# Kernel optimization log

Measured on AMD Instinct MI355X. Metric: run time of the kernel, lower is better.

## Reference

```python
import jax, jax.numpy as jnp
import numpy as np

N_NODES = 100000
N_EDGES = 1600000
NUM_GRAPHS = 128


def _gcn_layer(x, W, b, senders, receivers, n_node):
    # Linear transform first (cheaper: feature dim small)
    x = x @ W + b  # [N, out]
    ones = jnp.ones(senders.shape[0], dtype=x.dtype)
    deg_s = jax.ops.segment_sum(ones, senders, n_node)     # out-degree
    deg_r = jax.ops.segment_sum(ones, receivers, n_node)   # in-degree
    # symmetric normalization: D^-1/2 A D^-1/2
    x = x * jax.lax.rsqrt(jnp.maximum(deg_s, 1.0))[:, None]
    x = jax.ops.segment_sum(x[senders], receivers, n_node)  # gather-scatter aggregation
    x = x * jax.lax.rsqrt(jnp.maximum(deg_r, 1.0))[:, None]
    return x


def setup_inputs() -> dict:
    key = jax.random.key(0)
    ks = jax.random.split(key, 10)
    x = jax.random.normal(ks[0], (N_NODES, 9), dtype=jnp.float32)
    senders = jax.random.randint(ks[1], (N_EDGES,), 0, N_NODES)
    receivers = jax.random.randint(ks[2], (N_EDGES,), 0, N_NODES)
    batch = jnp.sort(jax.random.randint(ks[3], (N_NODES,), 0, NUM_GRAPHS))
    # learned params (Dense: W [in,out], b [out]) with LeCun-normal-ish scale
    def dense(k, din, dout):
        return jax.random.normal(k, (din, dout), dtype=jnp.float32) / np.sqrt(din)
    W1 = dense(ks[4], 9, 64)
    b1 = jnp.zeros((64,), jnp.float32)
    W2 = dense(ks[5], 64, 128)
    b2 = jnp.zeros((128,), jnp.float32)
    W3 = dense(ks[6], 128, 2)
    b3 = jnp.zeros((2,), jnp.float32)
    return {"x": x, "senders": senders, "receivers": receivers, "batch": batch,
            "num_graphs": NUM_GRAPHS, "W1": W1, "b1": b1, "W2": W2, "b2": b2,
            "W3": W3, "b3": b3}


def reference(x, senders, receivers, batch, num_graphs, W1, b1, W2, b2, W3, b3):
    n_node = x.shape[0]
    x = jax.nn.relu(_gcn_layer(x, W1, b1, senders, receivers, n_node))
    x = jax.nn.relu(_gcn_layer(x, W2, b2, senders, receivers, n_node))
    x = _gcn_layer(x, W3, b3, senders, receivers, n_node)
    # graph-level pooling
    return jax.ops.segment_sum(x, batch, num_graphs)
```

## Files before the change

### kernel.cpp

```cpp
#include <hip/hip_runtime.h>
#include <hip/hip_bf16.h>
#include <cstddef>

#define NBMAX 512
#define BCAP 5120
#define BKCHUNK 3200

typedef unsigned short bf16t;
typedef __attribute__((ext_vector_type(8))) short short8;
typedef __attribute__((ext_vector_type(4))) float f32x4;

static __device__ __forceinline__ float2 up2(unsigned u) {
    return make_float2(__uint_as_float(u << 16), __uint_as_float(u & 0xffff0000u));
}
static __device__ __forceinline__ bf16t f2bf(float f) {
    unsigned u = __float_as_uint(f);
    u += 0x7fffu + ((u >> 16) & 1u);
    return (bf16t)(u >> 16);
}
static __device__ __forceinline__ unsigned pk2(float a, float b) {
    return (unsigned)f2bf(a) | ((unsigned)f2bf(b) << 16);
}

__global__ void k_bucket(const int* __restrict__ S, const int* __restrict__ R,
                         unsigned* __restrict__ bufR, unsigned char* __restrict__ bufS,
                         int* __restrict__ gCntR, int* __restrict__ gCntS,
                         const float* __restrict__ W2, bf16t* __restrict__ W2f,
                         int nE, int nB) {
    __shared__ int histR[NBMAX], lstR[NBMAX], baseR[NBMAX];
    __shared__ int histS[NBMAX], lstS[NBMAX], baseS[NBMAX];
    __shared__ int sm[256];
    __shared__ unsigned sortedR[BKCHUNK];
    __shared__ unsigned short bOfR[BKCHUNK];
    __shared__ unsigned char sortedS[BKCHUNK];
    __shared__ unsigned short bOfS[BKCHUNK];
    int t = threadIdx.x;
    int nSort = gridDim.x - 4;
    if (blockIdx.x >= nSort) {
        int tt = (blockIdx.x - nSort) * blockDim.x + t;
        if (tt < 1024) {
            int nt = tt >> 7, kh = (tt >> 6) & 1, lane = tt & 63;
            int n = nt * 16 + (lane & 15);
            int k0 = kh * 32 + (lane >> 4) * 8;
            uint4 p;
            p.x = pk2(W2[(k0 + 0) * 128 + n], W2[(k0 + 1) * 128 + n]);
            p.y = pk2(W2[(k0 + 2) * 128 + n], W2[(k0 + 3) * 128 + n]);
            p.z = pk2(W2[(k0 + 4) * 128 + n], W2[(k0 + 5) * 128 + n]);
            p.w = pk2(W2[(k0 + 6) * 128 + n], W2[(k0 + 7) * 128 + n]);
            ((uint4*)W2f)[tt] = p;
        }
        return;
    }
    for (int i = t; i < NBMAX; i += 256) { histR[i] = 0; histS[i] = 0; }
    __syncthreads();
    int chunk = (nE + nSort - 1) / nSort;
    int e0 = blockIdx.x * chunk;
    int e1 = min(e0 + chunk, nE);
    for (int e = e0 + t; e < e1; e += 256) {
        atomicAdd(&histR[R[e] >> 8], 1);
        atomicAdd(&histS[S[e] >> 8], 1);
    }
    __syncthreads();
    {
        int c0 = histR[2 * t], c1 = histR[2 * t + 1];
        int ps = c0 + c1;
        sm[t] = ps;
        __syncthreads();
        for (int off = 1; off < 256; off <<= 1) {
            int y = (t >= off) ? sm[t - off] : 0;
            __syncthreads();
            sm[t] += y;
            __syncthreads();
        }
        int ex = sm[t] - ps;
        lstR[2 * t] = ex;
        lstR[2 * t + 1] = ex + c0;
    }
    __syncthreads();
    {
        int c0 = histS[2 * t], c1 = histS[2 * t + 1];
        int ps = c0 + c1;
        sm[t] = ps;
        __syncthreads();
        for (int off = 1; off < 256; off <<= 1) {
            int y = (t >= off) ? sm[t - off] : 0;
            __syncthreads();
            sm[t] += y;
            __syncthreads();
        }
        int ex = sm[t] - ps;
        lstS[2 * t] = ex;
        lstS[2 * t + 1] = ex + c0;
    }
    __syncthreads();
    for (int i = t; i < nB; i += 256) {
        int cR = histR[i];
        baseR[i] = cR ? atomicAdd(&gCntR[i], cR) : 0;
        int cS = histS[i];
        baseS[i] = cS ? atomicAdd(&gCntS[i], cS) : 0;
    }
    for (int i = t; i < NBMAX; i += 256) { histR[i] = 0; histS[i] = 0; }
    __syncthreads();
    for (int e = e0 + t; e < e1; e += 256) {
        int r = R[e], s = S[e];
        int br = r >> 8;
        int p = lstR[br] + atomicAdd(&histR[br], 1);
        sortedR[p] = ((unsigned)(r & 255) << 24) | (unsigned)s;
        bOfR[p] = (unsigned short)br;
        int bs = s >> 8;
        int p2 = lstS[bs] + atomicAdd(&histS[bs], 1);
        sortedS[p2] = (unsigned char)(s & 255);
        bOfS[p2] = (unsigned short)bs;
    }
    __syncthreads();
    int cnt = e1 - e0;
    for (int i = t; i < cnt; i += 256) {
        int b = bOfR[i];
        int slot = baseR[b] + (i - lstR[b]);
        if (slot < BCAP) bufR[(size_t)b * BCAP + slot] = sortedR[i];
        int b2 = bOfS[i];
        int slot2 = baseS[b2] + (i - lstS[b2]);
        if (slot2 < BCAP) bufS[(size_t)b2 * BCAP + slot2] = sortedS[i];
    }
}

__global__ void k_pass2(const unsigned* __restrict__ bufR, const unsigned char* __restrict__ bufS,
                        const int* __restrict__ gCntR, const int* __restrict__ gCntS,
                        const float* __restrict__ x,
                        int* __restrict__ csr, int* __restrict__ cur, int* __restrict__ degR,
                        float* __restrict__ inv_r, float* __restrict__ inv_s,
                        bf16t* __restrict__ xs, int nN, int nB) {
    __shared__ int hist[256], incl[256], curs[256], histS[256];
    __shared__ int sm[256];
    __shared__ int gex[NBMAX];
    int t = threadIdx.x;
    int b = blockIdx.x;
    {
        int c0 = (2 * t < nB) ? gCntR[2 * t] : 0;
        int c1 = (2 * t + 1 < nB) ? gCntR[2 * t + 1] : 0;
        int ps = c0 + c1;
        sm[t] = ps;
        __syncthreads();
        for (int off = 1; off < 256; off <<= 1) {
            int y = (t >= off) ? sm[t - off] : 0;
            __syncthreads();
            sm[t] += y;
            __syncthreads();
        }
        int ex = sm[t] - ps;
        gex[2 * t] = ex;
        gex[2 * t + 1] = ex + c0;
    }
    hist[t] = 0; curs[t] = 0; histS[t] = 0;
    __syncthreads();
    int gb = gex[b];
    int cnt = gCntR[b];
    const unsigned* buf = bufR + (size_t)b * BCAP;
    for (int i = t; i < cnt; i += 256) atomicAdd(&hist[buf[i] >> 24], 1);
    __syncthreads();
    int v = hist[t];
    sm[t] = v;
    __syncthreads();
    for (int off = 1; off < 256; off <<= 1) {
        int y = (t >= off) ? sm[t - off] : 0;
        __syncthreads();
        sm[t] += y;
        __syncthreads();
    }
    incl[t] = sm[t];
    __syncthreads();
    int n0 = b << 8;
    int n = n0 + t;
    if (n < nN) {
        degR[n] = v;
        cur[n] = gb + incl[t];
        inv_r[n] = rsqrtf(fmaxf((float)v, 1.f));
    }
    for (int i = t; i < cnt; i += 256) {
        unsigned p = buf[i];
        int rl = p >> 24;
        int s = p & 0xFFFFFF;
        int pos = gb + (incl[rl] - hist[rl]) + atomicAdd(&curs[rl], 1);
        csr[pos] = s;
    }
    int cntS = gCntS[b];
    const unsigned char* bufs = bufS + (size_t)b * BCAP;
    for (int i = t; i < cntS; i += 256) atomicAdd(&histS[bufs[i]], 1);
    __syncthreads();
    if (n < nN) {
        float is = rsqrtf(fmaxf((float)histS[t], 1.f));
        inv_s[n] = is;
        float w[9];
#pragma unroll
        for (int k = 0; k < 9; k++) w[k] = x[(size_t)n * 9 + k] * is;
        uint4 pa, pb;
        pa.x = pk2(w[0], w[1]); pa.y = pk2(w[2], w[3]);
        pa.z = pk2(w[4], w[5]); pa.w = pk2(w[6], w[7]);
        pb.x = pk2(w[8], is);   pb.y = 0; pb.z = 0; pb.w = 0;
        uint4* o = (uint4*)(xs + (size_t)n * 16);
        o[0] = pa;
        o[1] = pb;
    }
}

__global__ void k_h1f(const unsigned* __restrict__ xs32, const float* __restrict__ W1,
                      const float* __restrict__ b1,
                      const int* __restrict__ csr, const int* __restrict__ cur,
                      const int* __restrict__ degR, const float* __restrict__ inv_r,
                      const float* __restrict__ inv_s,
                      bf16t* __restrict__ h1s, float* __restrict__ warr, int nN) {
    __shared__ float Wl[9 * 64];
    __shared__ float bl[64];
    for (int i = threadIdx.x; i < 9 * 64; i += blockDim.x) Wl[i] = W1[i];
    if (threadIdx.x < 64) bl[threadIdx.x] = b1[threadIdx.x];
    __syncthreads();
    int lane = threadIdx.x & 63;
    int wave = threadIdx.x >> 6;
    int n = blockIdx.x * 16 + wave * 4 + (lane >> 4);
    int ql = lane & 15;
    int g = ql >> 2;
    int f2 = ql & 3;
    int nc = min(n, nN - 1);
    int deg = degR[nc];
    int st = cur[nc] - deg;
    float4 A0 = {0.f, 0.f, 0.f, 0.f}, A1 = A0, A2 = A0, A3 = A0;
    int i = 0;
    for (; i + 16 <= deg; i += 16) {
        int ea = csr[st + i + g];
        int eb = csr[st + i + 4 + g];
        int ec = csr[st + i + 8 + g];
        int ed = csr[st + i + 12 + g];
        uint2 u0 = *(const uint2*)(xs32 + (size_t)ea * 8 + f2 * 2);
        uint2 u1 = *(const uint2*)(xs32 + (size_t)eb * 8 + f2 * 2);
        uint2 u2 = *(const uint2*)(xs32 + (size_t)ec * 8 + f2 * 2);
        uint2 u3 = *(const uint2*)(xs32 + (size_t)ed * 8 + f2 * 2);
        float2 a = up2(u0.x), b = up2(u0.y);
        A0.x += a.x; A0.y += a.y; A0.z += b.x; A0.w += b.y;
        a = up2(u1.x); b = up2(u1.y);
        A1.x += a.x; A1.y += a.y; A1.z += b.x; A1.w += b.y;
        a = up2(u2.x); b = up2(u2.y);
        A2.x += a.x; A2.y += a.y; A2.z += b.x; A2.w += b.y;
        a = up2(u3.x); b = up2(u3.y);
        A3.x += a.x; A3.y += a.y; A3.z += b.x; A3.w += b.y;
    }
    for (; i + 4 <= deg; i += 4) {
        int ea = csr[st + i + g];
        uint2 u0 = *(const uint2*)(xs32 + (size_t)ea * 8 + f2 * 2);
        float2 a = up2(u0.x), b = up2(u0.y);
        A0.x += a.x; A0.y += a.y; A0.z += b.x; A0.w += b.y;
    }
    if (g < deg - i) {
        int ea = csr[st + i + g];
        uint2 u0 = *(const uint2*)(xs32 + (size_t)ea * 8 + f2 * 2);
        float2 a = up2(u0.x), b = up2(u0.y);
        A1.x += a.x; A1.y += a.y; A1.z += b.x; A1.w += b.y;
    }
    float4 vq = {(A0.x + A1.x) + (A2.x + A3.x), (A0.y + A1.y) + (A2.y + A3.y),
                 (A0.z + A1.z) + (A2.z + A3.z), (A0.w + A1.w) + (A2.w + A3.w)};
    vq.x += __shfl_xor(vq.x, 4); vq.y += __shfl_xor(vq.y, 4);
    vq.z += __shfl_xor(vq.z, 4); vq.w += __shfl_xor(vq.w, 4);
    vq.x += __shfl_xor(vq.x, 8); vq.y += __shfl_xor(vq.y, 8);
    vq.z += __shfl_xor(vq.z, 8); vq.w += __shfl_xor(vq.w, 8);
    int base = lane & 48;
    float xv[9];
    xv[0] = __shfl(vq.x, base + 0); xv[1] = __shfl(vq.y, base + 0);
    xv[2] = __shfl(vq.z, base + 0); xv[3] = __shfl(vq.w, base + 0);
    xv[4] = __shfl(vq.x, base + 1); xv[5] = __shfl(vq.y, base + 1);
    xv[6] = __shfl(vq.z, base + 1); xv[7] = __shfl(vq.w, base + 1);
    xv[8] = __shfl(vq.x, base + 2);
    float w = __shfl(vq.y, base + 2);
    float ir = inv_r[nc];
    float is = inv_s[nc];
    int c0 = ql * 4;
    float acc[4];
#pragma unroll
    for (int j = 0; j < 4; j++) acc[j] = w * bl[c0 + j];
#pragma unroll
    for (int k = 0; k < 9; k++) {
        float4 wv = *(const float4*)(Wl + k * 64 + c0);
        acc[0] += xv[k] * wv.x;
        acc[1] += xv[k] * wv.y;
        acc[2] += xv[k] * wv.z;
        acc[3] += xv[k] * wv.w;
    }
    if (n < nN) {
        float v0 = fmaxf(acc[0] * ir, 0.f) * is;
        float v1 = fmaxf(acc[1] * ir, 0.f) * is;
        float v2 = fmaxf(acc[2] * ir, 0.f) * is;
        float v3 = fmaxf(acc[3] * ir, 0.f) * is;
        uint2 pv;
        pv.x = pk2(v0, v1);
        pv.y = pk2(v2, v3);
        *(uint2*)(h1s + (size_t)n * 64 + c0) = pv;
        if (ql == 0) warr[n] = w;
    }
}

__global__ void k_l2f(const unsigned* __restrict__ h32, const bf16t* __restrict__ W2f,
                      const float* __restrict__ b2, const float* __restrict__ W3,
                      const float* __restrict__ inv_r, const float* __restrict__ inv_s,
                      const float* __restrict__ warr,
                      const int* __restrict__ csr, const int* __restrict__ cur,
                      const int* __restrict__ degR,
                      float* __restrict__ t, float* __restrict__ dout, int outSize, int nN) {
    __shared__ float b2l[128];
    __shared__ float W3l[256];
    __shared__ unsigned zl[64 * 36];
    for (int i = threadIdx.x; i < 128; i += blockDim.x) b2l[i] = b2[i];
    for (int i = threadIdx.x; i < 256; i += blockDim.x) W3l[i] = W3[i];
    if (blockIdx.x == 0 && threadIdx.x < outSize) dout[threadIdx.x] = 0.f;
    int lane = threadIdx.x & 63;
    int wave = threadIdx.x >> 6;
    int n0w = blockIdx.x * 64 + wave * 16;
    int q = lane >> 4;
    int ql = lane & 15;
    for (int j = 0; j < 16; j++) {
        int nc = min(n0w + j, nN - 1);
        int deg = degR[nc];
        int st = cur[nc] - deg;
        float4 A0 = {0.f, 0.f, 0.f, 0.f}, A1 = A0, A2 = A0, A3 = A0;
        int i = 0;
        for (; i + 16 <= deg; i += 16) {
            int ea = csr[st + i + q];
            int eb = csr[st + i + 4 + q];
            int ec = csr[st + i + 8 + q];
            int ed = csr[st + i + 12 + q];
            uint2 u0 = *(const uint2*)(h32 + (size_t)ea * 32 + ql * 2);
            uint2 u1 = *(const uint2*)(h32 + (size_t)eb * 32 + ql * 2);
            uint2 u2 = *(const uint2*)(h32 + (size_t)ec * 32 + ql * 2);
            uint2 u3 = *(const uint2*)(h32 + (size_t)ed * 32 + ql * 2);
            float2 a = up2(u0.x), bb = up2(u0.y);
            A0.x += a.x; A0.y += a.y; A0.z += bb.x; A0.w += bb.y;
            a = up2(u1.x); bb = up2(u1.y);
            A1.x += a.x; A1.y += a.y; A1.z += bb.x; A1.w += bb.y;
            a = up2(u2.x); bb = up2(u2.y);
            A2.x += a.x; A2.y += a.y; A2.z += bb.x; A2.w += bb.y;
            a = up2(u3.x); bb = up2(u3.y);
            A3.x += a.x; A3.y += a.y; A3.z += bb.x; A3.w += bb.y;
        }
        for (; i + 4 <= deg; i += 4) {
            int ea = csr[st + i + q];
            uint2 u0 = *(const uint2*)(h32 + (size_t)ea * 32 + ql * 2);
            float2 a = up2(u0.x), bb = up2(u0.y);
            A0.x += a.x; A0.y += a.y; A0.z += bb.x; A0.w += bb.y;
        }
        if (q < deg - i) {
            int ea = csr[st + i + q];
            uint2 u0 = *(const uint2*)(h32 + (size_t)ea * 32 + ql * 2);
            float2 a = up2(u0.x), bb = up2(u0.y);
            A1.x += a.x; A1.y += a.y; A1.z += bb.x; A1.w += bb.y;
        }
        float4 v = {(A0.x + A1.x) + (A2.x + A3.x), (A0.y + A1.y) + (A2.y + A3.y),
                    (A0.z + A1.z) + (A2.z + A3.z), (A0.w + A1.w) + (A2.w + A3.w)};
        v.x += __shfl_xor(v.x, 16); v.y += __shfl_xor(v.y, 16);
        v.z += __shfl_xor(v.z, 16); v.w += __shfl_xor(v.w, 16);
        v.x += __shfl_xor(v.x, 32); v.y += __shfl_xor(v.y, 32);
        v.z += __shfl_xor(v.z, 32); v.w += __shfl_xor(v.w, 32);
        if (q == 0) {
            uint2 pv;
            pv.x = pk2(v.x, v.y);
            pv.y = pk2(v.z, v.w);
            *(uint2*)(zl + (wave * 16 + j) * 36 + ql * 2) = pv;
        }
    }
    __syncthreads();
    int m = ql;
    int row = wave * 16 + m;
    short8 afr0 = *(const short8*)(zl + row * 36 + q * 4);
    short8 afr1 = *(const short8*)(zl + row * 36 + 16 + q * 4);
    float w4[4], ir4[4], is4[4];
#pragma unroll
    for (int reg = 0; reg < 4; reg++) {
        int nr = min(n0w + q * 4 + reg, nN - 1);
        w4[reg] = warr[nr];
        ir4[reg] = inv_r[nr];
        is4[reg] = inv_s[nr];
    }
    float p0[4] = {0.f, 0.f, 0.f, 0.f}, p1[4] = {0.f, 0.f, 0.f, 0.f};
#pragma unroll
    for (int nt = 0; nt < 8; nt++) {
        short8 b0 = *(const short8*)(W2f + ((size_t)(nt * 2 + 0) * 64 + lane) * 8);
        short8 b1 = *(const short8*)(W2f + ((size_t)(nt * 2 + 1) * 64 + lane) * 8);
        f32x4 acc = {0.f, 0.f, 0.f, 0.f};
        acc = __builtin_amdgcn_mfma_f32_16x16x32_bf16(afr0, b0, acc, 0, 0, 0);
        acc = __builtin_amdgcn_mfma_f32_16x16x32_bf16(afr1, b1, acc, 0, 0, 0);
        int col = nt * 16 + m;
        float bc = b2l[col];
        float w30 = W3l[col * 2 + 0];
        float w31 = W3l[col * 2 + 1];
#pragma unroll
        for (int reg = 0; reg < 4; reg++) {
            float h = fmaxf((acc[reg] + w4[reg] * bc) * ir4[reg], 0.f) * is4[reg];
            p0[reg] += h * w30;
            p1[reg] += h * w31;
        }
    }
#pragma unroll
    for (int mask = 1; mask < 16; mask <<= 1) {
#pragma unroll
        for (int reg = 0; reg < 4; reg++) {
            p0[reg] += __shfl_xor(p0[reg], mask);
            p1[reg] += __shfl_xor(p1[reg], mask);
        }
    }
    if (m == 0) {
#pragma unroll
        for (int reg = 0; reg < 4; reg++) {
            int nr = n0w + q * 4 + reg;
            if (nr < nN) *(float2*)(t + (size_t)nr * 2) = make_float2(p0[reg], p1[reg]);
        }
    }
}

__global__ void k_poolg(const float* __restrict__ t, const float* __restrict__ inv_r,
                        const float* __restrict__ warr, const float* __restrict__ b3,
                        const int* __restrict__ csr, const int* __restrict__ cur,
                        const int* __restrict__ degR, const int* __restrict__ batch,
                        float* out, int nN, int outSize) {
    __shared__ float sm[256];
    for (int i = threadIdx.x; i < 256; i += blockDim.x) sm[i] = 0.f;
    __syncthreads();
    float b30 = b3[0], b31 = b3[1];
    int n = blockIdx.x * blockDim.x + threadIdx.x;
    if (n < nN) {
        int deg = degR[n];
        int st = cur[n] - deg;
        float a0 = 0.f, a1 = 0.f, c0 = 0.f, c1 = 0.f;
        float d0 = 0.f, d1 = 0.f, e0 = 0.f, e1 = 0.f;
        int i = 0;
        for (; i + 4 <= deg; i += 4) {
            int sa = csr[st + i], sb = csr[st + i + 1];
            int sc = csr[st + i + 2], sd = csr[st + i + 3];
            float2 va = ((const float2*)t)[sa];
            float2 vb = ((const float2*)t)[sb];
            float2 vc = ((const float2*)t)[sc];
            float2 vd = ((const float2*)t)[sd];
            a0 += va.x; a1 += va.y;
            c0 += vb.x; c1 += vb.y;
            d0 += vc.x; d1 += vc.y;
            e0 += vd.x; e1 += vd.y;
        }
        for (; i < deg; i++) {
            float2 va = ((const float2*)t)[csr[st + i]];
            a0 += va.x; a1 += va.y;
        }
        float ir = inv_r[n];
        float wb = warr[n] * ir;
        int g = batch[n];
        atomicAdd(&sm[2 * g + 0], ((a0 + c0) + (d0 + e0)) * ir + wb * b30);
        atomicAdd(&sm[2 * g + 1], ((a1 + c1) + (d1 + e1)) * ir + wb * b31);
    }
    __syncthreads();
    for (int i = threadIdx.x; i < outSize; i += blockDim.x) atomicAdd(&out[i], sm[i]);
}

extern "C" void kernel_launch(void* const* d_in, const int* in_sizes, int n_in,
                              void* d_out, int out_size, void* d_ws, size_t ws_size,
                              hipStream_t stream) {
    const float* x     = (const float*)d_in[0];
    const int*   S     = (const int*)d_in[1];
    const int*   R     = (const int*)d_in[2];
    const int*   batch = (const int*)d_in[3];
    const float* W1 = (const float*)d_in[5];
    const float* b1 = (const float*)d_in[6];
    const float* W2 = (const float*)d_in[7];
    const float* b2 = (const float*)d_in[8];
    const float* W3 = (const float*)d_in[9];
    const float* b3 = (const float*)d_in[10];

    int nN = in_sizes[0] / 9;
    int nE = in_sizes[1];
    int nB = (nN + 255) / 256;

    char* ws = (char*)d_ws;
    int*   cur   = (int*)ws;
    int*   degR  = cur + nN;
    float* inv_s = (float*)(degR + nN);
    float* inv_r = inv_s + nN;
    float* warr  = inv_r + nN;
    int*   gCntR = (int*)(warr + nN);
    int*   gCntS = gCntR + NBMAX;
    int*   csr   = gCntS + NBMAX;
    bf16t* xs    = (bf16t*)(csr + nE);
    bf16t* W2f   = xs + (size_t)nN * 16;
    char*  regA  = (char*)(W2f + 8192);
    unsigned*      bufR = (unsigned*)regA;
    unsigned char* bufS = (unsigned char*)(bufR + (size_t)NBMAX * BCAP);
    bf16t* h1s = (bf16t*)regA;
    float* t   = (float*)(regA + (size_t)NBMAX * BCAP * 5);

    const int B = 256;

    hipMemsetAsync(gCntR, 0, 2 * NBMAX * 4, stream);
    k_bucket<<<516, B, 0, stream>>>(S, R, bufR, bufS, gCntR, gCntS, W2, W2f, nE, nB);
    k_pass2<<<nB, B, 0, stream>>>(bufR, bufS, gCntR, gCntS, x, csr, cur, degR,
                                  inv_r, inv_s, xs, nN, nB);

    k_h1f<<<(nN + 15) / 16, B, 0, stream>>>((const unsigned*)xs, W1, b1, csr, cur, degR,
                                            inv_r, inv_s, h1s, warr, nN);

    k_l2f<<<(nN + 63) / 64, B, 0, stream>>>((const unsigned*)h1s, W2f, b2, W3,
                                            inv_r, inv_s, warr, csr, cur, degR,
                                            t, (float*)d_out, out_size, nN);

    k_poolg<<<(nN + B - 1) / B, B, 0, stream>>>(t, inv_r, warr, b3, csr, cur, degR, batch,
                                                (float*)d_out, nN, out_size);
}
```

Baseline: 228.1 us.

## Assign one node per quarter-wave in layer-2 gather instead of splitting edges

The layer-2 gather kernel now gives each 16-lane quarter-wave its own destination node and walks that node's edges serially, unrolled by four. Previously all four quarter-waves split one node's edges and combined them with cross-lane shuffles. This removes the shuffle reduction and the idle lanes on low-degree nodes, and exposes more independent loads per wave. Blocks shrink to 128 threads covering 32 nodes, with launch bounds set for higher occupancy. The trade-off is possible load imbalance between quarter-waves when node degrees differ, and divergent loop trip counts within a wave.

New measurement: 219.8 us. 1.04x faster.

```diff
diff --git a/kernel.cpp b/kernel.cpp
--- a/kernel.cpp
+++ b/kernel.cpp
@@ -296,35 +296,38 @@
     }
 }
 
-__global__ void k_l2f(const unsigned* __restrict__ h32, const bf16t* __restrict__ W2f,
-                      const float* __restrict__ b2, const float* __restrict__ W3,
-                      const float* __restrict__ inv_r, const float* __restrict__ inv_s,
-                      const float* __restrict__ warr,
-                      const int* __restrict__ csr, const int* __restrict__ cur,
-                      const int* __restrict__ degR,
-                      float* __restrict__ t, float* __restrict__ dout, int outSize, int nN) {
+__global__ void __launch_bounds__(128, 8)
+k_l2f(const unsigned* __restrict__ h32, const bf16t* __restrict__ W2f,
+      const float* __restrict__ b2, const float* __restrict__ W3,
+      const float* __restrict__ inv_r, const float* __restrict__ inv_s,
+      const float* __restrict__ warr,
+      const int* __restrict__ csr, const int* __restrict__ cur,
+      const int* __restrict__ degR,
+      float* __restrict__ t, float* __restrict__ dout, int outSize, int nN) {
     __shared__ float b2l[128];
     __shared__ float W3l[256];
-    __shared__ unsigned zl[64 * 36];
+    __shared__ unsigned zl[32 * 36];
     for (int i = threadIdx.x; i < 128; i += blockDim.x) b2l[i] = b2[i];
     for (int i = threadIdx.x; i < 256; i += blockDim.x) W3l[i] = W3[i];
-    if (blockIdx.x == 0 && threadIdx.x < outSize) dout[threadIdx.x] = 0.f;
+    if (blockIdx.x == 0)
+        for (int i = threadIdx.x; i < outSize; i += blockDim.x) dout[i] = 0.f;
     int lane = threadIdx.x & 63;
     int wave = threadIdx.x >> 6;
-    int n0w = blockIdx.x * 64 + wave * 16;
-    int q = lane >> 4;
+    int qw = lane >> 4;
     int ql = lane & 15;
-    for (int j = 0; j < 16; j++) {
-        int nc = min(n0w + j, nN - 1);
+    int n0w = blockIdx.x * 32 + wave * 16;
+    for (int j2 = 0; j2 < 4; j2++) {
+        int roff = qw * 4 + j2;
+        int nc = min(n0w + roff, nN - 1);
         int deg = degR[nc];
         int st = cur[nc] - deg;
         float4 A0 = {0.f, 0.f, 0.f, 0.f}, A1 = A0, A2 = A0, A3 = A0;
         int i = 0;
-        for (; i + 16 <= deg; i += 16) {
-            int ea = csr[st + i + q];
-            int eb = csr[st + i + 4 + q];
-            int ec = csr[st + i + 8 + q];
-            int ed = csr[st + i + 12 + q];
+        for (; i + 4 <= deg; i += 4) {
+            int ea = csr[st + i];
+            int eb = csr[st + i + 1];
+            int ec = csr[st + i + 2];
+            int ed = csr[st + i + 3];
             uint2 u0 = *(const uint2*)(h32 + (size_t)ea * 32 + ql * 2);
             uint2 u1 = *(const uint2*)(h32 + (size_t)eb * 32 + ql * 2);
             uint2 u2 = *(const uint2*)(h32 + (size_t)ec * 32 + ql * 2);
@@ -338,33 +341,36 @@
             a = up2(u3.x); bb = up2(u3.y);
             A3.x += a.x; A3.y += a.y; A3.z += bb.x; A3.w += bb.y;
         }
-        for (; i + 4 <= deg; i += 4) {
-            int ea = csr[st + i + q];
+        if (i < deg) {
+            int ea = csr[st + i];
             uint2 u0 = *(const uint2*)(h32 + (size_t)ea * 32 + ql * 2);
             float2 a = up2(u0.x), bb = up2(u0.y);
             A0.x += a.x; A0.y += a.y; A0.z += bb.x; A0.w += bb.y;
-        }
-        if (q < deg - i) {
-            int ea = csr[st + i + q];
+            i++;
+        }
+        if (i < deg) {
+            int ea = csr[st + i];
             uint2 u0 = *(const uint2*)(h32 + (size_t)ea * 32 + ql * 2);
             float2 a = up2(u0.x), bb = up2(u0.y);
             A1.x += a.x; A1.y += a.y; A1.z += bb.x; A1.w += bb.y;
+            i++;
+        }
+        if (i < deg) {
+            int ea = csr[st + i];
+            uint2 u0 = *(const uint2*)(h32 + (size_t)ea * 32 + ql * 2);
+            float2 a = up2(u0.x), bb = up2(u0.y);
+            A2.x += a.x; A2.y += a.y; A2.z += bb.x; A2.w += bb.y;
         }
         float4 v = {(A0.x + A1.x) + (A2.x + A3.x), (A0.y + A1.y) + (A2.y + A3.y),
                     (A0.z + A1.z) + (A2.z + A3.z), (A0.w + A1.w) + (A2.w + A3.w)};
-        v.x += __shfl_xor(v.x, 16); v.y += __shfl_xor(v.y, 16);
-        v.z += __shfl_xor(v.z, 16); v.w += __shfl_xor(v.w, 16);
-        v.x += __shfl_xor(v.x, 32); v.y += __shfl_xor(v.y, 32);
-        v.z += __shfl_xor(v.z, 32); v.w += __shfl_xor(v.w, 32);
-        if (q == 0) {
-            uint2 pv;
-            pv.x = pk2(v.x, v.y);
-            pv.y = pk2(v.z, v.w);
-            *(uint2*)(zl + (wave * 16 + j) * 36 + ql * 2) = pv;
-        }
+        uint2 pv;
+        pv.x = pk2(v.x, v.y);
+        pv.y = pk2(v.z, v.w);
+        *(uint2*)(zl + (wave * 16 + roff) * 36 + ql * 2) = pv;
     }
     __syncthreads();
     int m = ql;
+    int q = lane >> 4;
     int row = wave * 16 + m;
     short8 afr0 = *(const short8*)(zl + row * 36 + q * 4);
     short8 afr1 = *(const short8*)(zl + row * 36 + 16 + q * 4);
@@ -499,9 +505,9 @@
     k_h1f<<<(nN + 15) / 16, B, 0, stream>>>((const unsigned*)xs, W1, b1, csr, cur, degR,
                                             inv_r, inv_s, h1s, warr, nN);
 
-    k_l2f<<<(nN + 63) / 64, B, 0, stream>>>((const unsigned*)h1s, W2f, b2, W3,
-                                            inv_r, inv_s, warr, csr, cur, degR,
-                                            t, (float*)d_out, out_size, nN);
+    k_l2f<<<(nN + 31) / 32, 128, 0, stream>>>((const unsigned*)h1s, W2f, b2, W3,
+                                              inv_r, inv_s, warr, csr, cur, degR,
+                                              t, (float*)d_out, out_size, nN);
 
     k_poolg<<<(nN + B - 1) / B, B, 0, stream>>>(t, inv_r, warr, b3, csr, cur, degR, batch,
                                                 (float*)d_out, nN, out_size);
```
